# Optimization experiments

Measured on AMD Instinct MI355X. Metric: run time of the kernel, lower is better.

## Reference

```python
import jax, jax.numpy as jnp
import numpy as np

H = 16
ROPE_BASE = 10000.0

def _rope_cos_sin(seq_len, d_k, dtype):
    inv_freq = 1.0 / (ROPE_BASE ** (jnp.arange(0, d_k, 2, dtype=jnp.float32) / d_k))
    t = jnp.arange(seq_len, dtype=jnp.float32)
    freqs = jnp.einsum('s,d->sd', t, inv_freq)          # [S, d_k/2]
    emb = jnp.concatenate([freqs, freqs], axis=-1)       # [S, d_k]
    return jnp.cos(emb).astype(dtype), jnp.sin(emb).astype(dtype)

def _rotate_half(x):
    x1, x2 = jnp.split(x, 2, axis=-1)
    return jnp.concatenate([-x2, x1], axis=-1)

def setup_inputs() -> dict:
    key = jax.random.key(0)
    ks = jax.random.split(key, 11)
    B, S, D = 2, 2048, 1024
    sc = 0.02
    return {
        'query': jax.random.normal(ks[0], (B, S, D), jnp.float32),
        'key':   jax.random.normal(ks[1], (B, S, D), jnp.float32),
        'value': jax.random.normal(ks[2], (B, S, D), jnp.float32),
        'Wq': jax.random.normal(ks[3], (D, D), jnp.float32) * sc,
        'bq': jnp.zeros((D,), jnp.float32),
        'Wk': jax.random.normal(ks[4], (D, D), jnp.float32) * sc,
        'bk': jnp.zeros((D,), jnp.float32),
        'Wv': jax.random.normal(ks[5], (D, D), jnp.float32) * sc,
        'bv': jnp.zeros((D,), jnp.float32),
        'Wo': jax.random.normal(ks[6], (D, D), jnp.float32) * sc,
        'bo': jnp.zeros((D,), jnp.float32),
    }

def reference(query, key, value, Wq, bq, Wk, bk, Wv, bv, Wo, bo):
    B, S, D = query.shape
    d_k = D // H
    # QKV projections (torch Linear: x @ W.T + b), split heads -> [B, H, S, d_k]
    def proj(x, W, b):
        return (x @ W.T + b).reshape(B, S, H, d_k).transpose(0, 2, 1, 3)
    q = proj(query, Wq, bq)
    k = proj(key, Wk, bk)
    v = proj(value, Wv, bv)
    # Rotary position embedding applied to q and k
    cos, sin = _rope_cos_sin(S, d_k, q.dtype)            # [S, d_k]
    cos = cos[None, None, :, :]
    sin = sin[None, None, :, :]
    q = q * cos + _rotate_half(q) * sin
    k = k * cos + _rotate_half(k) * sin
    # Scaled dot-product attention
    scores = jnp.einsum('bhqd,bhkd->bhqk', q, k) / jnp.sqrt(jnp.asarray(d_k, q.dtype))
    attn = jax.nn.softmax(scores, axis=-1)
    x = jnp.einsum('bhqk,bhkd->bhqd', attn, v)           # [B, H, S, d_k]
    x = x.transpose(0, 2, 1, 3).reshape(B, S, D)
    return x @ Wo.T + bo
```

## Files before the change

kernel.cpp:

```cpp
#include <hip/hip_runtime.h>
#include <hip/hip_bf16.h>
#include <math.h>


#define B_ 2
#define S_ 2048
#define D_ 1024
#define H_ 16
#define DK 64

typedef __attribute__((ext_vector_type(8)))  __bf16    bf16x8;
typedef __attribute__((ext_vector_type(8)))  _Float16  f16x8;
typedef __attribute__((ext_vector_type(4)))  float     f32x4;
typedef __attribute__((ext_vector_type(16))) float     f32x16;
typedef __attribute__((ext_vector_type(8)))  unsigned short u16x8;
typedef __attribute__((ext_vector_type(4)))  unsigned short u16x4;

#if __has_builtin(__builtin_amdgcn_exp2f)
#define EXP2(x) __builtin_amdgcn_exp2f(x)
#else
#define EXP2(x) exp2f(x)
#endif

static __device__ __forceinline__ unsigned short f2bf(float x) {
    union { float f; unsigned u; } v; v.f = x;
    unsigned r = v.u + 0x7FFFu + ((v.u >> 16) & 1u);
    return (unsigned short)(r >> 16);
}
static __device__ __forceinline__ unsigned cvtpk(float lo, float hi) {
    unsigned r;
    asm("v_cvt_pk_bf16_f32 %0, %1, %2" : "=v"(r) : "v"(lo), "v"(hi));
    return r;
}
static __device__ __forceinline__ unsigned cvtpk16(float lo, float hi) {
    unsigned r;
    asm("v_cvt_pkrtz_f16_f32 %0, %1, %2" : "=v"(r) : "v"(lo), "v"(hi));
    return r;
}
static __device__ __forceinline__ void gload_lds16(const void* g, void* l) {
    __builtin_amdgcn_global_load_lds(
        (const __attribute__((address_space(1))) void*)g,
        (__attribute__((address_space(3))) void*)l, 16, 0, 0);
}
static __device__ __forceinline__ int swz(int R, int c) {
    return ((R >> 1) << 6) + (((((R & 1) << 2) | c) ^ ((R >> 1) & 7)) << 3);
}
static __device__ __forceinline__ void splitpk16(float e0, float e1,
                                                 unsigned& hd, unsigned& ld) {
    hd = cvtpk16(e0, e1);
    union { unsigned u; _Float16 h[2]; } t; t.u = hd;
    ld = cvtpk16(e0 - (float)t.h[0], e1 - (float)t.h[1]);
}

__global__ __launch_bounds__(256) void wsplit4(
    const float* __restrict__ W0, const float* __restrict__ W1,
    const float* __restrict__ W2, const float* __restrict__ W3,
    unsigned short* __restrict__ out)
{
    const int idx = blockIdx.x * 256 + threadIdx.x;
    const int t = idx >> 17;
    const size_t e = (size_t)(idx & 131071) * 8;
    const float* src = (t==0 ? W0 : t==1 ? W1 : t==2 ? W2 : W3) + e;
    float4 a = *(const float4*)src;
    float4 b = *(const float4*)(src + 4);
    float x[8] = {a.x,a.y,a.z,a.w,b.x,b.y,b.z,b.w};
    union { _Float16 h[8]; u16x8 v; } Hh;
    #pragma unroll
    for (int j = 0; j < 8; ++j) Hh.h[j] = (_Float16)x[j];
    *(u16x8*)(out + (size_t)t * 1048576 + e) = Hh.v;
}

__global__ __launch_bounds__(512) void trigemm(
    const float* __restrict__ Aq, const float* __restrict__ Ak,
    const float* __restrict__ Av, const unsigned short* __restrict__ wsp,
    const float* __restrict__ bq, const float* __restrict__ bk,
    const float* __restrict__ bv,
    unsigned short* __restrict__ qb, unsigned short* __restrict__ kb,
    unsigned short* __restrict__ vt)
{
    __shared__ __align__(16) char ldsb[32768];
    const int pid = blockIdx.z;
    const float* A    = (pid==0) ? Aq : (pid==1) ? Ak : Av;
    const float* bias = (pid==0) ? bq : (pid==1) ? bk : bv;
    const unsigned short* Whp = wsp + (size_t)pid * 1048576;

    const int tid = threadIdx.x;
    const int w = tid >> 6, lane = tid & 63;
    const int l15 = lane & 15, g4 = lane >> 4;
    const int wr = w >> 1, wc = w & 1;
    const int bx = blockIdx.x, by = blockIdx.y;

    const int arow = tid >> 2, ac = tid & 3;
    const float* gpA = A + (size_t)(bx*128 + arow) * 1024 + ac * 8;
    const int aoff = swz(arow, ac);

    const int sr_ = tid >> 3, slot_ = tid & 7;
    const int z_  = slot_ ^ (sr_ & 7);
    const int wR_ = sr_*2 + (z_ >> 2);
    const unsigned short* gpW = Whp + (size_t)(by*128 + wR_) * 1024 + (z_ & 3) * 8;

    f32x4 acc[2][4];
    #pragma unroll
    for (int m = 0; m < 2; ++m)
        #pragma unroll
        for (int n = 0; n < 4; ++n) acc[m][n] = (f32x4){0.f,0.f,0.f,0.f};

    {
        float4 p0 = *(const float4*)(gpA);
        float4 p1 = *(const float4*)(gpA + 4);
        gload_lds16(gpW, ldsb + 8192 + tid * 16);
        union { unsigned u[4]; u16x8 v; } hh;
        hh.u[0] = cvtpk16(p0.x, p0.y); hh.u[1] = cvtpk16(p0.z, p0.w);
        hh.u[2] = cvtpk16(p1.x, p1.y); hh.u[3] = cvtpk16(p1.z, p1.w);
        *(u16x8*)((unsigned short*)ldsb + aoff) = hh.v;
    }
    asm volatile("s_waitcnt vmcnt(0) lgkmcnt(0)" ::: "memory");
    __builtin_amdgcn_s_barrier();
    asm volatile("" ::: "memory");

    for (int t = 0; t < 32; ++t) {
        const int cur = t & 1;
        float4 n0, n1;
        if (t < 31) {
            n0 = *(const float4*)(gpA + (t+1)*32);
            n1 = *(const float4*)(gpA + (t+1)*32 + 4);
            gload_lds16(gpW + (size_t)(t+1)*32, ldsb + (cur^1)*16384 + 8192 + tid*16);
            asm volatile("s_waitcnt vmcnt(3)" ::: "memory");
        } else {
            asm volatile("s_waitcnt vmcnt(0)" ::: "memory");
        }
        __builtin_amdgcn_s_barrier();
        asm volatile("" ::: "memory");

        const unsigned short* Ab = (const unsigned short*)(ldsb + cur*16384);
        const unsigned short* Wb = Ab + 4096;
        f16x8 ah[2], wh4[4];
        #pragma unroll
        for (int m = 0; m < 2; ++m)
            ah[m] = *(const f16x8*)(Ab + swz(wr*32 + m*16 + l15, g4));
        #pragma unroll
        for (int n = 0; n < 4; ++n)
            wh4[n] = *(const f16x8*)(Wb + swz(wc*64 + n*16 + l15, g4));
        #pragma unroll
        for (int m = 0; m < 2; ++m)
            #pragma unroll
            for (int n = 0; n < 4; ++n)
                acc[m][n] = __builtin_amdgcn_mfma_f32_16x16x32_f16(ah[m], wh4[n], acc[m][n], 0,0,0);

        if (t < 31) {
            union { unsigned u[4]; u16x8 v; } hh;
            hh.u[0] = cvtpk16(n0.x, n0.y); hh.u[1] = cvtpk16(n0.z, n0.w);
            hh.u[2] = cvtpk16(n1.x, n1.y); hh.u[3] = cvtpk16(n1.z, n1.w);
            *(u16x8*)((unsigned short*)(ldsb + (cur^1)*16384) + aoff) = hh.v;
        }
        asm volatile("s_waitcnt lgkmcnt(0)" ::: "memory");
        __builtin_amdgcn_s_barrier();
        asm volatile("" ::: "memory");
    }

    const int colBase = by*128 + wc*64;
    const int rowBase = bx*128 + wr*32;
    const int h = colBase >> 6;

    if (pid < 2) {
        unsigned short* Out = pid ? kb : qb;
        const float QSC = pid ? 1.0f : 0.125f * 1.44269504088896340736f;
        #pragma unroll
        for (int m = 0; m < 2; ++m) {
            const int srow0 = rowBase + m*16 + g4*4;
            const int b = srow0 >> 11;
            unsigned short* hb2 = Out + (size_t)(b*H_ + h) * S_ * DK;
            #pragma unroll
            for (int n = 0; n < 2; ++n) {
                const int d = n*16 + l15;
                const float invf = exp2f((float)d * -0.4152410118609203f);
                const float b1 = bias[h*64 + d], b2 = bias[h*64 + d + 32];
                #pragma unroll
                for (int r = 0; r < 4; ++r) {
                    const int s = (srow0 + r) & 2047;
                    const float x1 = acc[m][n][r]   + b1;
                    const float x2 = acc[m][n+2][r] + b2;
                    float sn, cc;
                    __sincosf((float)s * invf, &sn, &cc);
                    const float o1 = (x1*cc - x2*sn) * QSC;
                    const float o2 = (x2*cc + x1*sn) * QSC;
                    if (pid == 0) {
                        unsigned short* dst = hb2 + (size_t)s * DK;
                        dst[d]      = f2bf(o1);
                        dst[d + 32] = f2bf(o2);
                    } else {
                        unsigned short* tb = hb2 + (s >> 6) * 4096 + (s & 63) * 8;
                        tb[(d >> 3) * 512 + (d & 7)]        = f2bf(o1);
                        tb[(d >> 3) * 512 + 2048 + (d & 7)] = f2bf(o2);
                    }
                }
            }
        }
    } else {
        #pragma unroll
        for (int m = 0; m < 2; ++m) {
            const int srow0 = rowBase + m*16 + g4*4;
            const int b = srow0 >> 11, s0 = srow0 & 2047;
            unsigned short* tb = vt + (size_t)(b*H_ + h) * S_ * DK
                               + (s0 >> 6) * 4096 + ((s0 & 63) >> 3) * 512 + (s0 & 7);
            #pragma unroll
            for (int n = 0; n < 4; ++n) {
                const int d = n*16 + l15;
                const float bb = bias[h*64 + d];
                u16x4 pk;
                #pragma unroll
                for (int r = 0; r < 4; ++r) pk[r] = f2bf(acc[m][n][r] + bb);
                *(u16x4*)(tb + d * 8) = pk;
            }
        }
    }
}

__global__ __launch_bounds__(512) void mfma_gemm0(
    const unsigned short* __restrict__ Ah, const unsigned short* __restrict__ Al,
    const unsigned short* __restrict__ Wh,
    const float* __restrict__ bias, float* __restrict__ Out)
{
    __shared__ __align__(16) char ldsb[49152];
    const int tid = threadIdx.x;
    const int w = tid >> 6, lane = tid & 63;
    const int l15 = lane & 15, g4 = lane >> 4;
    const int wr = w >> 1, wc = w & 1;
    const int bx = blockIdx.x, by = blockIdx.y;

    const int u_ = w >> 1, qq = w & 1;
    const unsigned short* gsrc = (u_==0) ? Ah : (u_==1) ? Al : Wh;
    const int row0 = (u_ < 2) ? bx * 128 : by * 128;
    const int lr8 = lane >> 3;
    const int zz  = (lane & 7) ^ lr8;
    const int wR0 = qq*64 + (lr8 << 1) + (zz >> 2);
    const unsigned short* gp0 = gsrc + (size_t)(row0 + wR0) * 1024 + (zz & 3) * 8;

    f32x4 acc[2][4];
    #pragma unroll
    for (int m = 0; m < 2; ++m)
        #pragma unroll
        for (int n = 0; n < 4; ++n) acc[m][n] = (f32x4){0.f,0.f,0.f,0.f};

    #define STAGE(T, BUF) do {                                              \
        if (w < 6) {                                                        \
            const unsigned short* g_ = gp0 + (size_t)(T) * 32;              \
            char* d_ = ldsb + (BUF)*24576 + u_*8192 + qq*4096;              \
            gload_lds16(g_,          d_);                                   \
            gload_lds16(g_ + 16384,  d_ + 1024);                            \
            gload_lds16(g_ + 32768,  d_ + 2048);                            \
            gload_lds16(g_ + 49152,  d_ + 3072);                            \
        }                                                                   \
    } while (0)

    STAGE(0, 0);
    asm volatile("s_waitcnt vmcnt(0)" ::: "memory");
    __builtin_amdgcn_s_barrier();
    asm volatile("" ::: "memory");

    for (int t = 0; t < 32; ++t) {
        const int cur = t & 1;
        if (t < 31) {
            STAGE(t + 1, cur ^ 1);
            asm volatile("s_waitcnt vmcnt(4)" ::: "memory");
        } else {
            asm volatile("s_waitcnt vmcnt(0)" ::: "memory");
        }
        __builtin_amdgcn_s_barrier();
        asm volatile("" ::: "memory");

        const unsigned short* Ahb = (const unsigned short*)(ldsb + cur*24576);
        const unsigned short* Alb = Ahb + 4096;
        const unsigned short* Whb = Ahb + 8192;

        f16x8 ah2[2], al2[2], wh4[4];
        #pragma unroll
        for (int m = 0; m < 2; ++m) {
            const int off = swz(wr*32 + m*16 + l15, g4);
            ah2[m] = *(const f16x8*)(Ahb + off);
            al2[m] = *(const f16x8*)(Alb + off);
        }
        #pragma unroll
        for (int n = 0; n < 4; ++n) {
            const int off = swz(wc*64 + n*16 + l15, g4);
            wh4[n] = *(const f16x8*)(Whb + off);
        }
        #pragma unroll
        for (int m = 0; m < 2; ++m)
            #pragma unroll
            for (int n = 0; n < 4; ++n) {
                acc[m][n] = __builtin_amdgcn_mfma_f32_16x16x32_f16(ah2[m], wh4[n], acc[m][n], 0,0,0);
                acc[m][n] = __builtin_amdgcn_mfma_f32_16x16x32_f16(al2[m], wh4[n], acc[m][n], 0,0,0);
            }

        asm volatile("" ::: "memory");
        __builtin_amdgcn_s_barrier();
        asm volatile("" ::: "memory");
    }
    #undef STAGE

    const int colBase = by*128 + wc*64;
    const int rowBase = bx*128 + wr*32;
    #pragma unroll
    for (int m = 0; m < 2; ++m) {
        const int row = rowBase + m*16 + g4*4;
        #pragma unroll
        for (int n = 0; n < 4; ++n) {
            const int col = colBase + n*16 + l15;
            const float bb = bias[col];
            #pragma unroll
            for (int r = 0; r < 4; ++r)
                Out[(size_t)(row + r) * 1024 + col] = acc[m][n][r] + bb;
        }
    }
}

__global__ __launch_bounds__(512, 1) void attn_mfma8(
    const unsigned short* __restrict__ Qb, const unsigned short* __restrict__ Kb,
    const unsigned short* __restrict__ Vt,
    unsigned short* __restrict__ Xh, unsigned short* __restrict__ Xl)
{
    __shared__ __align__(16) char lds[65536];
    const unsigned bid = blockIdx.x;
    const int xcd = bid & 7, idx = bid >> 3;
    const int bh  = xcd * 4 + (idx >> 3);
    const int qt  = idx & 7;
    const int tid = threadIdx.x;
    const int w = tid >> 6, lane = tid & 63;
    const int l31 = lane & 31, hi = lane >> 5;
    const size_t bhO = (size_t)bh * S_ * DK;
    const int q0 = qt * 256 + w * 32;

    const int u0   = w * 4;
    const int isV  = u0 >> 4;
    const int u15  = u0 & 15;
    const int su0  = u15 >> 3;
    const unsigned short* sb = (isV ? Vt : Kb) + bhO;
    const int ch0 = u15 & 7;
    char* const dbase = lds;

    bf16x8 qf[4];
    #pragma unroll
    for (int ks = 0; ks < 4; ++ks)
        qf[ks] = *(const bf16x8*)(Qb + bhO + (size_t)(q0 + l31) * DK + ks*16 + hi*8);

    f32x16 oT[2];
    #pragma unroll
    for (int dh = 0; dh < 2; ++dh)
        #pragma unroll
        for (int r = 0; r < 16; ++r) oT[dh][r] = 0.f;
    float l_ = 0.f;

    #define ASTAGE(T, BUF) do {                                                     \
        const unsigned short* g_ = sb + (size_t)((T)*2 + su0) * 4096 + ch0 * 512    \
                                   + lane * 8;                                      \
        char* d_ = dbase + (BUF)*32768 + isV*16384 + su0*8192 + ch0*1024 + lane*16; \
        gload_lds16(g_,         d_);                                                \
        gload_lds16(g_ + 512,   d_ + 1024);                                         \
        gload_lds16(g_ + 1024,  d_ + 2048);                                         \
        gload_lds16(g_ + 1536,  d_ + 3072);                                         \
    } while (0)

    ASTAGE(0, 0);
    asm volatile("s_waitcnt vmcnt(0)" ::: "memory");
    __builtin_amdgcn_s_barrier();
    asm volatile("" ::: "memory");

    for (int t = 0; t < 16; ++t) {
        const int cur = t & 1;
        if (t < 15) {
            ASTAGE(t + 1, cur ^ 1);
            asm volatile("s_waitcnt vmcnt(4)" ::: "memory");
        } else {
            asm volatile("s_waitcnt vmcnt(0)" ::: "memory");
        }
        __builtin_amdgcn_s_barrier();
        asm volatile("" ::: "memory");

        const char* Kl = lds + cur * 32768;
        const char* Vl = Kl + 16384;

        f32x16 s2[4];
        __builtin_amdgcn_s_setprio(1);
        #pragma unroll
        for (int kb2 = 0; kb2 < 4; ++kb2) {
            f32x16 a;
            #pragma unroll
            for (int r = 0; r < 16; ++r) a[r] = 0.f;
            const char* kbase = Kl + (kb2 >> 1) * 8192 + ((kb2 & 1) * 32 + l31) * 16;
            #pragma unroll
            for (int ks = 0; ks < 4; ++ks) {
                bf16x8 kf = *(const bf16x8*)(kbase + (ks*2 + hi) * 1024);
                a = __builtin_amdgcn_mfma_f32_32x32x16_bf16(kf, qf[ks], a, 0, 0, 0);
            }
            s2[kb2] = a;
        }
        __builtin_amdgcn_s_setprio(0);

        {
            float lsum = 0.f;
            #pragma unroll
            for (int kb2 = 0; kb2 < 4; ++kb2)
                #pragma unroll
                for (int r = 0; r < 16; ++r) {
                    const float p = EXP2(s2[kb2][r]);
                    s2[kb2][r] = p; lsum += p;
                }
            l_ += lsum;
        }

        #pragma unroll
        for (int ks2 = 0; ks2 < 8; ++ks2) {
            const int kb2 = ks2 >> 1;
            const int R0  = (ks2 & 1) * 8;
            unsigned a0 = cvtpk(s2[kb2][R0+0], s2[kb2][R0+1]);
            unsigned a1 = cvtpk(s2[kb2][R0+2], s2[kb2][R0+3]);
            unsigned b0 = cvtpk(s2[kb2][R0+4], s2[kb2][R0+5]);
            unsigned b1 = cvtpk(s2[kb2][R0+6], s2[kb2][R0+7]);
            asm("v_permlane32_swap_b32 %0, %1" : "+v"(a0), "+v"(b0));
            asm("v_permlane32_swap_b32 %0, %1" : "+v"(a1), "+v"(b1));
            union { unsigned u[4]; bf16x8 v; } pf;
            pf.u[0] = a0; pf.u[1] = a1; pf.u[2] = b0; pf.u[3] = b1;
            const char* vbase = Vl + (ks2 >> 2) * 8192 + (((ks2 & 3) * 2) + hi) * 1024;
            __builtin_amdgcn_s_setprio(1);
            #pragma unroll
            for (int dh = 0; dh < 2; ++dh) {
                bf16x8 vf = *(const bf16x8*)(vbase + (dh*32 + l31) * 16);
                oT[dh] = __builtin_amdgcn_mfma_f32_32x32x16_bf16(vf, pf.v, oT[dh], 0, 0, 0);
            }
            __builtin_amdgcn_s_setprio(0);
        }

        asm volatile("" ::: "memory");
        __builtin_amdgcn_s_barrier();
        asm volatile("" ::: "memory");
    }
    #undef ASTAGE

    l_ += __shfl_xor(l_, 32, 64);
    const float inv = 1.0f / l_;
    const int b = bh >> 4, h = bh & 15;
    const int q = q0 + l31;
    unsigned short* xh = Xh + (((size_t)b * S_ + q) * H_ + h) * DK;
    unsigned short* xl = Xl + (((size_t)b * S_ + q) * H_ + h) * DK;
    #pragma unroll
    for (int dh = 0; dh < 2; ++dh)
        #pragma unroll
        for (int tt = 0; tt < 4; ++tt) {
            const int dk0 = dh*32 + tt*8 + hi*4;
            const float o0 = oT[dh][tt*4 + 0] * inv;
            const float o1 = oT[dh][tt*4 + 1] * inv;
            const float o2 = oT[dh][tt*4 + 2] * inv;
            const float o3 = oT[dh][tt*4 + 3] * inv;
            union { unsigned u[2]; u16x4 v; } hv, lv;
            splitpk16(o0, o1, hv.u[0], lv.u[0]);
            splitpk16(o2, o3, hv.u[1], lv.u[1]);
            *(u16x4*)(xh + dk0) = hv.v;
            *(u16x4*)(xl + dk0) = lv.v;
        }
}

extern "C" void kernel_launch(void* const* d_in, const int* in_sizes, int n_in,
                              void* d_out, int out_size, void* d_ws, size_t ws_size,
                              hipStream_t stream)
{
    const float* query = (const float*)d_in[0];
    const float* key   = (const float*)d_in[1];
    const float* value = (const float*)d_in[2];
    const float* Wq = (const float*)d_in[3];  const float* bq = (const float*)d_in[4];
    const float* Wk = (const float*)d_in[5];  const float* bk = (const float*)d_in[6];
    const float* Wv = (const float*)d_in[7];  const float* bv = (const float*)d_in[8];
    const float* Wo = (const float*)d_in[9];  const float* bo = (const float*)d_in[10];
    float* out = (float*)d_out;

    char* ws = (char*)d_ws;
    const size_t MB = (size_t)1 << 20;
    unsigned short* Xh  = (unsigned short*)(ws + 0*MB);
    unsigned short* Xl  = (unsigned short*)(ws + 8*MB);
    unsigned short* qb  = (unsigned short*)(ws + 16*MB);
    unsigned short* vt  = (unsigned short*)(ws + 24*MB);
    unsigned short* kb  = (unsigned short*)(ws + 40*MB);
    unsigned short* wsp = (unsigned short*)(ws + 48*MB);
    unsigned short* Woh = wsp + 3145728;

    wsplit4<<<2048, 256, 0, stream>>>(Wq, Wk, Wv, Wo, wsp);

    trigemm<<<dim3(32, 8, 3), 512, 0, stream>>>(query, key, value, wsp,
                                                bq, bk, bv, qb, kb, vt);

    attn_mfma8<<<256, 512, 0, stream>>>(qb, kb, vt, Xh, Xl);

    mfma_gemm0<<<dim3(32, 8), 512, 0, stream>>>(Xh, Xl, Woh, bo, out);
}
```

Before: 118.3 us.

## Split attention KV range across two blocks, combine partials, drop low-half output GEMM

Attention now launches twice as many blocks, each covering half of the key/value sequence and writing unnormalized fp32 partial outputs plus row sums. A new combine kernel adds the two partials, normalizes, and writes an fp16 activation. The output GEMM drops the hi/lo fp16 split of the activation, halving its MFMA work and LDS traffic at some precision cost. The split relies on a fixed softmax offset rather than a per-row running max, since the halves are summed without rescaling. It adds fp32 partial traffic and an extra kernel launch, and reuses the output buffer as scratch.

Measured after the change: 122.5 us. 1.04x slower.

```diff
diff --git a/kernel.cpp b/kernel.cpp
--- a/kernel.cpp
+++ b/kernel.cpp
@@ -44,12 +44,6 @@
 }
 static __device__ __forceinline__ int swz(int R, int c) {
     return ((R >> 1) << 6) + (((((R & 1) << 2) | c) ^ ((R >> 1) & 7)) << 3);
-}
-static __device__ __forceinline__ void splitpk16(float e0, float e1,
-                                                 unsigned& hd, unsigned& ld) {
-    hd = cvtpk16(e0, e1);
-    union { unsigned u; _Float16 h[2]; } t; t.u = hd;
-    ld = cvtpk16(e0 - (float)t.h[0], e1 - (float)t.h[1]);
 }
 
 __global__ __launch_bounds__(256) void wsplit4(
@@ -216,120 +210,23 @@
     }
 }
 
-__global__ __launch_bounds__(512) void mfma_gemm0(
-    const unsigned short* __restrict__ Ah, const unsigned short* __restrict__ Al,
-    const unsigned short* __restrict__ Wh,
-    const float* __restrict__ bias, float* __restrict__ Out)
-{
-    __shared__ __align__(16) char ldsb[49152];
-    const int tid = threadIdx.x;
-    const int w = tid >> 6, lane = tid & 63;
-    const int l15 = lane & 15, g4 = lane >> 4;
-    const int wr = w >> 1, wc = w & 1;
-    const int bx = blockIdx.x, by = blockIdx.y;
-
-    const int u_ = w >> 1, qq = w & 1;
-    const unsigned short* gsrc = (u_==0) ? Ah : (u_==1) ? Al : Wh;
-    const int row0 = (u_ < 2) ? bx * 128 : by * 128;
-    const int lr8 = lane >> 3;
-    const int zz  = (lane & 7) ^ lr8;
-    const int wR0 = qq*64 + (lr8 << 1) + (zz >> 2);
-    const unsigned short* gp0 = gsrc + (size_t)(row0 + wR0) * 1024 + (zz & 3) * 8;
-
-    f32x4 acc[2][4];
-    #pragma unroll
-    for (int m = 0; m < 2; ++m)
-        #pragma unroll
-        for (int n = 0; n < 4; ++n) acc[m][n] = (f32x4){0.f,0.f,0.f,0.f};
-
-    #define STAGE(T, BUF) do {                                              \
-        if (w < 6) {                                                        \
-            const unsigned short* g_ = gp0 + (size_t)(T) * 32;              \
-            char* d_ = ldsb + (BUF)*24576 + u_*8192 + qq*4096;              \
-            gload_lds16(g_,          d_);                                   \
-            gload_lds16(g_ + 16384,  d_ + 1024);                            \
-            gload_lds16(g_ + 32768,  d_ + 2048);                            \
-            gload_lds16(g_ + 49152,  d_ + 3072);                            \
-        }                                                                   \
-    } while (0)
-
-    STAGE(0, 0);
-    asm volatile("s_waitcnt vmcnt(0)" ::: "memory");
-    __builtin_amdgcn_s_barrier();
-    asm volatile("" ::: "memory");
-
-    for (int t = 0; t < 32; ++t) {
-        const int cur = t & 1;
-        if (t < 31) {
-            STAGE(t + 1, cur ^ 1);
-            asm volatile("s_waitcnt vmcnt(4)" ::: "memory");
-        } else {
-            asm volatile("s_waitcnt vmcnt(0)" ::: "memory");
-        }
-        __builtin_amdgcn_s_barrier();
-        asm volatile("" ::: "memory");
-
-        const unsigned short* Ahb = (const unsigned short*)(ldsb + cur*24576);
-        const unsigned short* Alb = Ahb + 4096;
-        const unsigned short* Whb = Ahb + 8192;
-
-        f16x8 ah2[2], al2[2], wh4[4];
-        #pragma unroll
-        for (int m = 0; m < 2; ++m) {
-            const int off = swz(wr*32 + m*16 + l15, g4);
-            ah2[m] = *(const f16x8*)(Ahb + off);
-            al2[m] = *(const f16x8*)(Alb + off);
-        }
-        #pragma unroll
-        for (int n = 0; n < 4; ++n) {
-            const int off = swz(wc*64 + n*16 + l15, g4);
-            wh4[n] = *(const f16x8*)(Whb + off);
-        }
-        #pragma unroll
-        for (int m = 0; m < 2; ++m)
-            #pragma unroll
-            for (int n = 0; n < 4; ++n) {
-                acc[m][n] = __builtin_amdgcn_mfma_f32_16x16x32_f16(ah2[m], wh4[n], acc[m][n], 0,0,0);
-                acc[m][n] = __builtin_amdgcn_mfma_f32_16x16x32_f16(al2[m], wh4[n], acc[m][n], 0,0,0);
-            }
-
-        asm volatile("" ::: "memory");
-        __builtin_amdgcn_s_barrier();
-        asm volatile("" ::: "memory");
-    }
-    #undef STAGE
-
-    const int colBase = by*128 + wc*64;
-    const int rowBase = bx*128 + wr*32;
-    #pragma unroll
-    for (int m = 0; m < 2; ++m) {
-        const int row = rowBase + m*16 + g4*4;
-        #pragma unroll
-        for (int n = 0; n < 4; ++n) {
-            const int col = colBase + n*16 + l15;
-            const float bb = bias[col];
-            #pragma unroll
-            for (int r = 0; r < 4; ++r)
-                Out[(size_t)(row + r) * 1024 + col] = acc[m][n][r] + bb;
-        }
-    }
-}
-
-__global__ __launch_bounds__(512, 1) void attn_mfma8(
+__global__ __launch_bounds__(512, 1) void attn_mfma9(
     const unsigned short* __restrict__ Qb, const unsigned short* __restrict__ Kb,
     const unsigned short* __restrict__ Vt,
-    unsigned short* __restrict__ Xh, unsigned short* __restrict__ Xl)
+    float* __restrict__ P0, float* __restrict__ P1, float* __restrict__ lbuf)
 {
     __shared__ __align__(16) char lds[65536];
     const unsigned bid = blockIdx.x;
     const int xcd = bid & 7, idx = bid >> 3;
-    const int bh  = xcd * 4 + (idx >> 3);
-    const int qt  = idx & 7;
+    const int bh   = xcd * 4 + (idx >> 4);
+    const int qt   = (idx >> 1) & 7;
+    const int half = idx & 1;
     const int tid = threadIdx.x;
     const int w = tid >> 6, lane = tid & 63;
     const int l31 = lane & 31, hi = lane >> 5;
     const size_t bhO = (size_t)bh * S_ * DK;
     const int q0 = qt * 256 + w * 32;
+    const int t0 = half * 8;
 
     const int u0   = w * 4;
     const int isV  = u0 >> 4;
@@ -361,15 +258,15 @@
         gload_lds16(g_ + 1536,  d_ + 3072);                                         \
     } while (0)
 
-    ASTAGE(0, 0);
+    ASTAGE(t0, 0);
     asm volatile("s_waitcnt vmcnt(0)" ::: "memory");
     __builtin_amdgcn_s_barrier();
     asm volatile("" ::: "memory");
 
-    for (int t = 0; t < 16; ++t) {
+    for (int t = 0; t < 8; ++t) {
         const int cur = t & 1;
-        if (t < 15) {
-            ASTAGE(t + 1, cur ^ 1);
+        if (t < 7) {
+            ASTAGE(t0 + t + 1, cur ^ 1);
             asm volatile("s_waitcnt vmcnt(4)" ::: "memory");
         } else {
             asm volatile("s_waitcnt vmcnt(0)" ::: "memory");
@@ -438,26 +335,130 @@
     #undef ASTAGE
 
     l_ += __shfl_xor(l_, 32, 64);
-    const float inv = 1.0f / l_;
     const int b = bh >> 4, h = bh & 15;
     const int q = q0 + l31;
-    unsigned short* xh = Xh + (((size_t)b * S_ + q) * H_ + h) * DK;
-    unsigned short* xl = Xl + (((size_t)b * S_ + q) * H_ + h) * DK;
+    float* P = half ? P1 : P0;
+    float* op = P + ((((size_t)b * S_ + q) * H_ + h) * DK);
+    if (hi == 0) lbuf[half * 65536 + (bh << 11) + q] = l_;
     #pragma unroll
     for (int dh = 0; dh < 2; ++dh)
         #pragma unroll
         for (int tt = 0; tt < 4; ++tt) {
             const int dk0 = dh*32 + tt*8 + hi*4;
-            const float o0 = oT[dh][tt*4 + 0] * inv;
-            const float o1 = oT[dh][tt*4 + 1] * inv;
-            const float o2 = oT[dh][tt*4 + 2] * inv;
-            const float o3 = oT[dh][tt*4 + 3] * inv;
-            union { unsigned u[2]; u16x4 v; } hv, lv;
-            splitpk16(o0, o1, hv.u[0], lv.u[0]);
-            splitpk16(o2, o3, hv.u[1], lv.u[1]);
-            *(u16x4*)(xh + dk0) = hv.v;
-            *(u16x4*)(xl + dk0) = lv.v;
-        }
+            float4 st = { oT[dh][tt*4+0], oT[dh][tt*4+1],
+                          oT[dh][tt*4+2], oT[dh][tt*4+3] };
+            *(float4*)(op + dk0) = st;
+        }
+}
+
+__global__ __launch_bounds__(256) void combine(
+    const float* __restrict__ P0, const float* __restrict__ P1,
+    const float* __restrict__ lbuf, unsigned short* __restrict__ Xh)
+{
+    const int gid = blockIdx.x * 256 + threadIdx.x;
+    const size_t e = (size_t)gid * 8;
+    const int h = (gid >> 3) & 15, s = (gid >> 7) & 2047, b = gid >> 18;
+    const int qidx = ((b * 16 + h) << 11) | s;
+    const float inv = 1.0f / (lbuf[qidx] + lbuf[65536 + qidx]);
+    float4 a0 = *(const float4*)(P0 + e);
+    float4 a1 = *(const float4*)(P0 + e + 4);
+    float4 c0 = *(const float4*)(P1 + e);
+    float4 c1 = *(const float4*)(P1 + e + 4);
+    float x[8] = { (a0.x+c0.x)*inv, (a0.y+c0.y)*inv, (a0.z+c0.z)*inv, (a0.w+c0.w)*inv,
+                   (a1.x+c1.x)*inv, (a1.y+c1.y)*inv, (a1.z+c1.z)*inv, (a1.w+c1.w)*inv };
+    union { _Float16 hh[8]; u16x8 v; } o;
+    #pragma unroll
+    for (int j = 0; j < 8; ++j) o.hh[j] = (_Float16)x[j];
+    *(u16x8*)(Xh + e) = o.v;
+}
+
+__global__ __launch_bounds__(512) void mfma_gemm0(
+    const unsigned short* __restrict__ Ah, const unsigned short* __restrict__ Wh,
+    const float* __restrict__ bias, float* __restrict__ Out)
+{
+    __shared__ __align__(16) char ldsb[32768];
+    const int tid = threadIdx.x;
+    const int w = tid >> 6, lane = tid & 63;
+    const int l15 = lane & 15, g4 = lane >> 4;
+    const int wr = w >> 1, wc = w & 1;
+    const int bx = blockIdx.x, by = blockIdx.y;
+
+    const int ten = (w >> 1) & 1, qq = w & 1;
+    const unsigned short* gsrc = ten ? Wh : Ah;
+    const int row0 = ten ? by * 128 : bx * 128;
+    const int lr8 = lane >> 3;
+    const int zz  = (lane & 7) ^ lr8;
+    const int wR0 = qq*64 + (lr8 << 1) + (zz >> 2);
+    const unsigned short* gp0 = gsrc + (size_t)(row0 + wR0) * 1024 + (zz & 3) * 8;
+
+    f32x4 acc[2][4];
+    #pragma unroll
+    for (int m = 0; m < 2; ++m)
+        #pragma unroll
+        for (int n = 0; n < 4; ++n) acc[m][n] = (f32x4){0.f,0.f,0.f,0.f};
+
+    #define STAGE(T, BUF) do {                                              \
+        if (w < 4) {                                                        \
+            const unsigned short* g_ = gp0 + (size_t)(T) * 32;              \
+            char* d_ = ldsb + (BUF)*16384 + ten*8192 + qq*4096;             \
+            gload_lds16(g_,          d_);                                   \
+            gload_lds16(g_ + 16384,  d_ + 1024);                            \
+            gload_lds16(g_ + 32768,  d_ + 2048);                            \
+            gload_lds16(g_ + 49152,  d_ + 3072);                            \
+        }                                                                   \
+    } while (0)
+
+    STAGE(0, 0);
+    asm volatile("s_waitcnt vmcnt(0)" ::: "memory");
+    __builtin_amdgcn_s_barrier();
+    asm volatile("" ::: "memory");
+
+    for (int t = 0; t < 32; ++t) {
+        const int cur = t & 1;
+        if (t < 31) {
+            STAGE(t + 1, cur ^ 1);
+            asm volatile("s_waitcnt vmcnt(4)" ::: "memory");
+        } else {
+            asm volatile("s_waitcnt vmcnt(0)" ::: "memory");
+        }
+        __builtin_amdgcn_s_barrier();
+        asm volatile("" ::: "memory");
+
+        const unsigned short* Ahb = (const unsigned short*)(ldsb + cur*16384);
+        const unsigned short* Whb = Ahb + 4096;
+        f16x8 ah2[2], wh4[4];
+        #pragma unroll
+        for (int m = 0; m < 2; ++m)
+            ah2[m] = *(const f16x8*)(Ahb + swz(wr*32 + m*16 + l15, g4));
+        #pragma unroll
+        for (int n = 0; n < 4; ++n)
+            wh4[n] = *(const f16x8*)(Whb + swz(wc*64 + n*16 + l15, g4));
+        #pragma unroll
+        for (int m = 0; m < 2; ++m)
+            #pragma unroll
+            for (int n = 0; n < 4; ++n)
+                acc[m][n] = __builtin_amdgcn_mfma_f32_16x16x32_f16(ah2[m], wh4[n], acc[m][n], 0,0,0);
+
+        asm volatile("" ::: "memory");
+        __builtin_amdgcn_s_barrier();
+        asm volatile("" ::: "memory");
+    }
+    #undef STAGE
+
+    const int colBase = by*128 + wc*64;
+    const int rowBase = bx*128 + wr*32;
+    #pragma unroll
+    for (int m = 0; m < 2; ++m) {
+        const int row = rowBase + m*16 + g4*4;
+        #pragma unroll
+        for (int n = 0; n < 4; ++n) {
+            const int col = colBase + n*16 + l15;
+            const float bb = bias[col];
+            #pragma unroll
+            for (int r = 0; r < 4; ++r)
+                Out[(size_t)(row + r) * 1024 + col] = acc[m][n][r] + bb;
+        }
+    }
 }
 
 extern "C" void kernel_launch(void* const* d_in, const int* in_sizes, int n_in,
@@ -475,20 +476,24 @@
 
     char* ws = (char*)d_ws;
     const size_t MB = (size_t)1 << 20;
-    unsigned short* Xh  = (unsigned short*)(ws + 0*MB);
-    unsigned short* Xl  = (unsigned short*)(ws + 8*MB);
-    unsigned short* qb  = (unsigned short*)(ws + 16*MB);
-    unsigned short* vt  = (unsigned short*)(ws + 24*MB);
-    unsigned short* kb  = (unsigned short*)(ws + 40*MB);
-    unsigned short* wsp = (unsigned short*)(ws + 48*MB);
-    unsigned short* Woh = wsp + 3145728;
+    float*          P0   = (float*)(ws + 0*MB);
+    unsigned short* qb   = (unsigned short*)(ws + 16*MB);
+    unsigned short* vt   = (unsigned short*)(ws + 24*MB);
+    float*          lbuf = (float*)(ws + 32*MB);
+    unsigned short* kb   = (unsigned short*)(ws + 40*MB);
+    unsigned short* XhF  = (unsigned short*)(ws + 40*MB);
+    unsigned short* wsp  = (unsigned short*)(ws + 48*MB);
+    unsigned short* Woh  = wsp + 3145728;
+    float*          P1   = out;
 
     wsplit4<<<2048, 256, 0, stream>>>(Wq, Wk, Wv, Wo, wsp);
 
     trigemm<<<dim3(32, 8, 3), 512, 0, stream>>>(query, key, value, wsp,
                                                 bq, bk, bv, qb, kb, vt);
 
-    attn_mfma8<<<256, 512, 0, stream>>>(qb, kb, vt, Xh, Xl);
-
-    mfma_gemm0<<<dim3(32, 8), 512, 0, stream>>>(Xh, Xl, Woh, bo, out);
-}
+    attn_mfma9<<<512, 512, 0, stream>>>(qb, kb, vt, P0, P1, lbuf);
+
+    combine<<<2048, 256, 0, stream>>>(P0, P1, lbuf, XhF);
+
+    mfma_gemm0<<<dim3(32, 8), 512, 0, stream>>>(XhF, Woh, bo, out);
+}
```
